# Kernel optimization log

Hardware: AMD Instinct MI355X
Metric: run time of the kernel (lower is better)

Reference implementation:

```python
import jax, jax.numpy as jnp
import numpy as np

B, L, HID = 2, 2048, 2560
H, HKV, DH = 32, 8, 128
G = H // HKV  # GQA groups = 4
EPS = 1e-6
THETA = 1000000.0


def setup_inputs() -> dict:
    key = jax.random.key(0)
    ks = jax.random.split(key, 6)
    x = jax.random.normal(ks[0], (B, L, HID), dtype=jnp.float32)
    Wq = jax.random.normal(ks[1], (HID, H * DH), dtype=jnp.float32) * 0.02
    Wk = jax.random.normal(ks[2], (HID, HKV * DH), dtype=jnp.float32) * 0.02
    Wv = jax.random.normal(ks[3], (HID, HKV * DH), dtype=jnp.float32) * 0.02
    Wo = jax.random.normal(ks[4], (H * DH, HID), dtype=jnp.float32) * 0.02
    q_norm_w = jnp.ones((DH,), dtype=jnp.float32)
    k_norm_w = jnp.ones((DH,), dtype=jnp.float32)
    # RoPE tables, theta=1e6, non-interleaved (half-split) layout
    inv_freq = 1.0 / (THETA ** (jnp.arange(0, DH, 2, dtype=jnp.float32) / DH))
    pos = jnp.arange(L, dtype=jnp.float32)
    freqs = pos[:, None] * inv_freq[None, :]              # [L, DH/2]
    emb = jnp.concatenate([freqs, freqs], axis=-1)        # [L, DH]
    cos = jnp.broadcast_to(jnp.cos(emb)[None], (B, L, DH))
    sin = jnp.broadcast_to(jnp.sin(emb)[None], (B, L, DH))
    return {"x": x, "Wq": Wq, "Wk": Wk, "Wv": Wv, "Wo": Wo,
            "q_norm_w": q_norm_w, "k_norm_w": k_norm_w,
            "cos": cos, "sin": sin}


def _rmsnorm(x, w):
    xf = x.astype(jnp.float32)
    var = jnp.mean(xf * xf, axis=-1, keepdims=True)
    return (xf * jax.lax.rsqrt(var + EPS)).astype(x.dtype) * w


def _rotate_half(x):
    x1, x2 = jnp.split(x, 2, axis=-1)
    return jnp.concatenate([-x2, x1], axis=-1)


def reference(x, Wq, Wk, Wv, Wo, q_norm_w, k_norm_w, cos, sin):
    b, l, _ = x.shape
    q = (x @ Wq).reshape(b, l, H, DH)
    k = (x @ Wk).reshape(b, l, HKV, DH)
    v = (x @ Wv).reshape(b, l, HKV, DH).transpose(0, 2, 1, 3)   # [B,HKV,L,DH]
    q = _rmsnorm(q, q_norm_w).transpose(0, 2, 1, 3)             # [B,H,L,DH]
    k = _rmsnorm(k, k_norm_w).transpose(0, 2, 1, 3)             # [B,HKV,L,DH]
    c = cos[:, None]  # [B,1,L,DH]
    s = sin[:, None]
    q = q * c + _rotate_half(q) * s
    k = k * c + _rotate_half(k) * s
    # GQA SDPA, causal
    qg = q.reshape(b, HKV, G, l, DH)
    scale = 1.0 / np.sqrt(DH)
    scores = jnp.einsum('bkgqd,bkmd->bkgqm', qg, k) * scale     # [B,HKV,G,L,L]
    causal = jnp.tril(jnp.ones((l, l), dtype=bool))
    scores = jnp.where(causal, scores, jnp.finfo(scores.dtype).min)
    attn = jax.nn.softmax(scores, axis=-1)
    out = jnp.einsum('bkgqm,bkmd->bkgqd', attn, v)              # [B,HKV,G,L,DH]
    out = out.reshape(b, H, l, DH).transpose(0, 2, 1, 3).reshape(b, l, H * DH)
    return out @ Wo
```

## Files before the change

kernel.cpp:

```cpp
#include <hip/hip_runtime.h>

typedef unsigned short u16;
typedef unsigned int u32;
using bf16x8 = __attribute__((ext_vector_type(8))) __bf16;
using f32x4  = __attribute__((ext_vector_type(4))) float;

typedef const void __attribute__((address_space(1)))* gas1p;
typedef void __attribute__((address_space(3)))* las3p;

__device__ __forceinline__ void gload16(const void* g, void* l) {
  __builtin_amdgcn_global_load_lds((gas1p)g, (las3p)l, 16, 0, 0);
}

__device__ __forceinline__ u16 f2bf(float f) {
  union { float f; unsigned u; } v; v.f = f;
  unsigned r = v.u + 0x7FFFu + ((v.u >> 16) & 1u);
  return (u16)(r >> 16);
}
__device__ __forceinline__ float bf2f(u16 h) {
  union { unsigned u; float f; } v; v.u = ((unsigned)h) << 16;
  return v.f;
}

__global__ __launch_bounds__(256)
void cvt_f32_bf16(const float4* __restrict__ in, uint2* __restrict__ out, int n4) {
  int i = blockIdx.x * 256 + threadIdx.x;
  if (i >= n4) return;
  float4 v = in[i];
  uint2 o;
  o.x = (unsigned)f2bf(v.x) | ((unsigned)f2bf(v.y) << 16);
  o.y = (unsigned)f2bf(v.z) | ((unsigned)f2bf(v.w) << 16);
  out[i] = o;
}

__global__ __launch_bounds__(256)
void transpose_w(const float* __restrict__ in, u16* __restrict__ out, int R, int C) {
  __shared__ float tile[32][33];
  const int tx = threadIdx.x & 31, ty = threadIdx.x >> 5;
  const int r0 = blockIdx.y * 32, c0 = blockIdx.x * 32;
#pragma unroll
  for (int i = 0; i < 4; i++)
    tile[ty + i * 8][tx] = in[(size_t)(r0 + ty + i * 8) * C + c0 + tx];
  __syncthreads();
#pragma unroll
  for (int i = 0; i < 4; i++)
    out[(size_t)(c0 + ty + i * 8) * R + r0 + tx] = f2bf(tile[tx][ty + i * 8]);
}

__global__ __launch_bounds__(256)
void transpose_v(const u16* __restrict__ QKV, u16* __restrict__ Vt) {
  __shared__ u16 tile[32][34];
  const int tx = threadIdx.x & 31, ty = threadIdx.x >> 5;
  const int l0 = blockIdx.x * 32, d0 = blockIdx.y * 32;
  const int bkv = blockIdx.z;
  const int b = bkv >> 3, kvh = bkv & 7;
#pragma unroll
  for (int i = 0; i < 4; i++)
    tile[ty + i * 8][tx] =
        QKV[(size_t)(b * 2048 + l0 + ty + i * 8) * 6144 + 5120 + kvh * 128 + d0 + tx];
  __syncthreads();
#pragma unroll
  for (int i = 0; i < 4; i++)
    Vt[((size_t)bkv * 128 + d0 + ty + i * 8) * 2048 + l0 + tx] = tile[tx][ty + i * 8];
}

__global__ __launch_bounds__(256)
void norm_rope(const u16* __restrict__ QKV, const float* __restrict__ qw,
               const float* __restrict__ kw, const float* __restrict__ cosp,
               const float* __restrict__ sinp, u16* __restrict__ Qr,
               u16* __restrict__ Kr) {
  const int rid = blockIdx.x * 4 + (threadIdx.x >> 6);
  const int lane = threadIdx.x & 63;
  const int head = rid % 40;
  const int bl = rid / 40;
  const int b = bl >> 11, l = bl & 2047;
  const u16* src; const float* w; u16* dst; float scale;
  if (head < 32) {
    src = QKV + (size_t)bl * 6144 + head * 128;
    w = qw;
    dst = Qr + ((size_t)(b * 32 + head) * 2048 + l) * 128;
    scale = 0.08838834764831845f;
  } else {
    const int kvh = head - 32;
    src = QKV + (size_t)bl * 6144 + 4096 + kvh * 128;
    w = kw;
    dst = Kr + ((size_t)(b * 8 + kvh) * 2048 + l) * 128;
    scale = 1.0f;
  }
  float lo = bf2f(src[lane]);
  float hi = bf2f(src[lane + 64]);
  float ss = lo * lo + hi * hi;
#pragma unroll
  for (int m = 1; m < 64; m <<= 1) ss += __shfl_xor(ss, m, 64);
  const float rstd = rsqrtf(ss * (1.0f / 128.0f) + 1e-6f) * scale;
  const float nlo = lo * rstd * w[lane];
  const float nhi = hi * rstd * w[lane + 64];
  const float* cb = cosp + (size_t)bl * 128;
  const float* sb = sinp + (size_t)bl * 128;
  dst[lane]      = f2bf(nlo * cb[lane]      - nhi * sb[lane]);
  dst[lane + 64] = f2bf(nhi * cb[lane + 64] + nlo * sb[lane + 64]);
}

#define BAR __builtin_amdgcn_s_barrier()
#define WLG { asm volatile("s_waitcnt lgkmcnt(0)" ::: "memory");            \
              __builtin_amdgcn_sched_barrier(0); }
#define WVMn(n) asm volatile("s_waitcnt vmcnt(" #n ")" ::: "memory")
#define SP1 __builtin_amdgcn_s_setprio(1)
#define SP0 __builtin_amdgcn_s_setprio(0)

template <int MI, int NJ, typename CT>
__global__ __launch_bounds__(512, 4)
void gemmK32(const u16* __restrict__ A, const u16* __restrict__ Bt,
             CT* __restrict__ C, int N, int K, int MT) {
  extern __shared__ char smem[];
  constexpr int ASZ = MI * 4096;
  constexpr int BSZ = NJ * 2048;
  constexpr int J1 = (MI == 4) ? 2 : 3;
  const int tid = threadIdx.x, lane = tid & 63, wid = tid >> 6;
  const int wm = wid >> 1, wn = wid & 1;
  const int fr = lane & 15, fq = lane >> 4;
  const int qx = (int)gridDim.x >> 3;
  const int wg = ((int)blockIdx.x & 7) * qx + ((int)blockIdx.x >> 3);
  const int bx = wg / MT, by = wg - bx * MT;
  const int m0 = by * (MI * 64), n0 = bx * (NJ * 32);
  const u16* Ab = A + (size_t)m0 * K;
  const u16* Bb = Bt + (size_t)n0 * K;

  char* const A0 = smem;
  char* const B0 = smem + 2 * ASZ;
#define ABUF(c) (A0 + (c) * ASZ)
#define BBUF(c) (B0 + (c) * BSZ)

  const int sF = (tid >> 2) * K + (tid & 3) * 8;
  const int tq = tid & 255;
  const int sH = (tq >> 2) * K + (tq & 3) * 8;
  const int to = tid & 127;
  const int sO = (to >> 2) * K + (to & 3) * 8;

  const int aRd = (wm * MI * 16 + fr) * 64 + fq * 16;
  const int bRd = (wn * 16 + fr) * 64 + fq * 16;

  f32x4 acc[MI][NJ];
#pragma unroll
  for (int i = 0; i < MI; i++)
#pragma unroll
    for (int j = 0; j < NJ; j++)
#pragma unroll
      for (int r = 0; r < 4; r++) acc[i][j][r] = 0.f;

  bf16x8 af[MI], bfr[3];
  const int NT = K >> 5;

  auto stageP1 = [&](int c2, int kk) {
    if constexpr (MI == 4) {
      gload16(Ab + sF + kk, ABUF(c2) + (tid << 4));
      gload16(Ab + sF + (size_t)128 * K + kk, ABUF(c2) + 8192 + (tid << 4));
    } else {
      gload16(Ab + sF + kk, ABUF(c2) + (tid << 4));
      gload16(Bb + sF + kk, BBUF(c2) + (tid << 4));
    }
  };
  auto stageP2 = [&](int c2, int kk) {
    if constexpr (MI == 4) {
      gload16(Bb + sH + kk, BBUF(c2) + (tq << 4));
      gload16(Bb + sH + (size_t)64 * K + kk, BBUF(c2) + 4096 + (tq << 4));
    } else {
      gload16(Bb + sO + (size_t)128 * K + kk, BBUF(c2) + 8192 + (to << 4));
    }
  };

  stageP1(0, 0);
  stageP2(0, 0);
  WVMn(1);
  BAR;

  for (int t = 0; t < NT; t++) {
    const int c = t & 1, cn = c ^ 1;
    const int kn = ((t + 1 == NT) ? 0 : (t + 1)) << 5;
#pragma unroll
    for (int i = 0; i < MI; i++)
      af[i] = *(const bf16x8*)(ABUF(c) + aRd + i * 1024);
#pragma unroll
    for (int j = 0; j < J1; j++)
      bfr[j] = *(const bf16x8*)(BBUF(c) + bRd + j * 2048);
    stageP1(cn, kn);
    WVMn(2);
    BAR; WLG; SP1;
#pragma unroll
    for (int j = 0; j < J1; j++)
#pragma unroll
      for (int i = 0; i < MI; i++)
        acc[i][j] = __builtin_amdgcn_mfma_f32_16x16x32_bf16(af[i], bfr[j], acc[i][j], 0, 0, 0);
    SP0; BAR;
#pragma unroll
    for (int j = J1; j < NJ; j++)
      bfr[j - J1] = *(const bf16x8*)(BBUF(c) + bRd + j * 2048);
    stageP2(cn, kn);
    WVMn(1);
    BAR; WLG; SP1;
#pragma unroll
    for (int j = J1; j < NJ; j++)
#pragma unroll
      for (int i = 0; i < MI; i++)
        acc[i][j] = __builtin_amdgcn_mfma_f32_16x16x32_bf16(af[i], bfr[j - J1], acc[i][j], 0, 0, 0);
    SP0; BAR;
  }
  WVMn(0);

#pragma unroll
  for (int i = 0; i < MI; i++) {
    const int row0 = m0 + (wm * MI + i) * 16 + fq * 4;
#pragma unroll
    for (int j = 0; j < NJ; j++) {
      const int col = n0 + (j * 2 + wn) * 16 + fr;
#pragma unroll
      for (int r = 0; r < 4; r++) {
        const size_t idx = (size_t)(row0 + r) * N + col;
        if constexpr (sizeof(CT) == 2) C[idx] = f2bf(acc[i][j][r]);
        else C[idx] = acc[i][j][r];
      }
    }
  }
#undef ABUF
#undef BBUF
}

__global__ __launch_bounds__(256, 2)
void attn_fwd(const u16* __restrict__ Qr, const u16* __restrict__ Kr,
              const u16* __restrict__ Vt, u16* __restrict__ AO) {
  const int L = 2048, DH = 128;
  __shared__ u16 Ks[2][64 * 128];
  __shared__ u16 Vs[2][128 * 64];
  const int tid = threadIdx.x, lane = tid & 63, wid = tid >> 6;
  const int fr = lane & 15, fq = lane >> 4;
  const int j = blockIdx.x >> 4;
  const int grp = blockIdx.x & 15;
  const int kvh = grp >> 1, b = grp & 1;
  const int h = kvh * 4 + wid;

  const u16* Kbase = Kr + (size_t)(b * 8 + kvh) * L * DH;
  const u16* Vbase = Vt + (size_t)(b * 8 + kvh) * DH * L;

  int Dly[4], kOff[4], vOff[4];
#pragma unroll
  for (int p = 0; p < 4; p++) {
    const int D = (tid + p * 256) * 16;
    Dly[p] = D;
    const int kr = D >> 8, kc = ((D >> 4) & 15) ^ (kr & 7);
    kOff[p] = kr * 128 + kc * 8;
    const int vr = D >> 7, vc = ((D >> 4) & 7) ^ (vr & 7);
    vOff[p] = vr * 2048 + vc * 8;
  }

  const bool B5 = (lane & 32) != 0;
  const bool A4 = (lane & 16) != 0;

  auto stage = [&](int kt, int bufi) {
    const int k0 = kt * 64;
#pragma unroll
    for (int p = 0; p < 4; p++) {
      gload16(Kbase + (size_t)k0 * 128 + kOff[p], (char*)&Ks[bufi][0] + Dly[p]);
      gload16(Vbase + k0 + vOff[p], (char*)&Vs[bufi][0] + Dly[p]);
    }
  };

  for (int half = 0; half < 2; half++) {
    const int t = half ? 63 - j : j;
    const int nk = (t >> 1) + 1;

    bf16x8 qf[2][4];
#pragma unroll
    for (int g = 0; g < 2; g++) {
      const int qq = t * 32 + g * 16 + fr;
      const u16* qbase = Qr + ((size_t)(b * 32 + h) * L + qq) * DH + fq * 8;
#pragma unroll
      for (int dt = 0; dt < 4; dt++) qf[g][dt] = *(const bf16x8*)(qbase + dt * 32);
    }
    asm volatile("s_waitcnt vmcnt(0)" ::: "memory");

    f32x4 o[2][8];
#pragma unroll
    for (int g = 0; g < 2; g++)
#pragma unroll
      for (int d = 0; d < 8; d++)
#pragma unroll
        for (int r = 0; r < 4; r++) o[g][d][r] = 0.f;
    float mrow[2] = {-__builtin_huge_valf(), -__builtin_huge_valf()};
    float lrow[2] = {0.f, 0.f};

    __builtin_amdgcn_s_barrier();
    stage(0, 0);
    int cur = 0;

    for (int kt = 0; kt < nk; kt++) {
      if (kt + 1 < nk) {
        stage(kt + 1, cur ^ 1);
        asm volatile("s_waitcnt vmcnt(8)" ::: "memory");
      } else {
        asm volatile("s_waitcnt vmcnt(0)" ::: "memory");
      }
      __builtin_amdgcn_s_barrier();

      const u16* KsB = &Ks[cur][0];
      const u16* VsB = &Vs[cur][0];
      const int k0 = kt * 64;

      f32x4 s4[2][4];
#pragma unroll
      for (int g = 0; g < 2; g++)
#pragma unroll
        for (int ni = 0; ni < 4; ni++)
#pragma unroll
          for (int r = 0; r < 4; r++) s4[g][ni][r] = 0.f;
#pragma unroll
      for (int ni = 0; ni < 4; ni++) {
        const int krow = ni * 16 + fr;
        const int sw = (krow & 7) << 4;
#pragma unroll
        for (int dt = 0; dt < 4; dt++) {
          const int off = (krow * 256 + dt * 64 + fq * 16) ^ sw;
          bf16x8 kf = *(const bf16x8*)((const char*)KsB + off);
          s4[0][ni] = __builtin_amdgcn_mfma_f32_16x16x32_bf16(kf, qf[0][dt], s4[0][ni], 0, 0, 0);
          s4[1][ni] = __builtin_amdgcn_mfma_f32_16x16x32_bf16(kf, qf[1][dt], s4[1][ni], 0, 0, 0);
        }
      }

      if (kt == nk - 1) {
#pragma unroll
        for (int g = 0; g < 2; g++) {
          const int qq = t * 32 + g * 16 + fr;
#pragma unroll
          for (int ni = 0; ni < 4; ni++)
#pragma unroll
            for (int r = 0; r < 4; r++)
              if (k0 + ni * 16 + fq * 4 + r > qq) s4[g][ni][r] = -1e30f;
        }
      }

      bf16x8 pb[2][2];
#pragma unroll
      for (int g = 0; g < 2; g++) {
        float mt = s4[g][0][0];
#pragma unroll
        for (int ni = 0; ni < 4; ni++)
#pragma unroll
          for (int r = 0; r < 4; r++) mt = fmaxf(mt, s4[g][ni][r]);
        mt = fmaxf(mt, __shfl_xor(mt, 16, 64));
        mt = fmaxf(mt, __shfl_xor(mt, 32, 64));

        if (!__all(mt <= mrow[g] + 8.f)) {
          const float mn = fmaxf(mrow[g], mt);
          const float corr = exp2f((mrow[g] - mn) * 1.44269504f);
          mrow[g] = mn;
          lrow[g] *= corr;
#pragma unroll
          for (int d = 0; d < 8; d++)
#pragma unroll
            for (int r = 0; r < 4; r++) o[g][d][r] *= corr;
        }

        const float ml = mrow[g] * 1.44269504f;
        float rs = 0.f;
#pragma unroll
        for (int ni = 0; ni < 4; ni++)
#pragma unroll
          for (int r = 0; r < 4; r++) {
            const float pv = exp2f(fmaf(s4[g][ni][r], 1.44269504f, -ml));
            s4[g][ni][r] = pv;
            rs += pv;
          }
        rs += __shfl_xor(rs, 16, 64);
        rs += __shfl_xor(rs, 32, 64);
        lrow[g] += rs;

        u32 pk[4][2];
#pragma unroll
        for (int ni = 0; ni < 4; ni++) {
          pk[ni][0] = __builtin_amdgcn_perm(__float_as_uint(s4[g][ni][1]),
                                            __float_as_uint(s4[g][ni][0]), 0x07060302u);
          pk[ni][1] = __builtin_amdgcn_perm(__float_as_uint(s4[g][ni][3]),
                                            __float_as_uint(s4[g][ni][2]), 0x07060302u);
        }
#pragma unroll
        for (int ks = 0; ks < 2; ks++) {
          u32 r00 = pk[2 * ks + 0][0], r01 = pk[2 * ks + 0][1];
          u32 r10 = pk[2 * ks + 1][0], r11 = pk[2 * ks + 1][1];
          u32 e0 = __shfl_xor(B5 ? r00 : r10, 32, 64);
          u32 t00 = B5 ? e0 : r00, t10 = B5 ? r10 : e0;
          u32 e1 = __shfl_xor(B5 ? r01 : r11, 32, 64);
          u32 t01 = B5 ? e1 : r01, t11 = B5 ? r11 : e1;
          u32 e2 = __shfl_xor(A4 ? t00 : t10, 16, 64);
          u32 u00 = A4 ? e2 : t00, u10 = A4 ? t10 : e2;
          u32 e3 = __shfl_xor(A4 ? t01 : t11, 16, 64);
          u32 u01 = A4 ? e3 : t01, u11 = A4 ? t11 : e3;
          union { u32 u[4]; bf16x8 v; } pbv;
          pbv.u[0] = u00; pbv.u[1] = u01; pbv.u[2] = u10; pbv.u[3] = u11;
          pb[g][ks] = pbv.v;
        }
      }

#pragma unroll
      for (int d = 0; d < 8; d++) {
        const int vrow = d * 16 + fr;
        const int sw = (vrow & 7) << 4;
#pragma unroll
        for (int ks = 0; ks < 2; ks++) {
          const int off = (vrow * 128 + ks * 64 + fq * 16) ^ sw;
          bf16x8 vf = *(const bf16x8*)((const char*)VsB + off);
          o[0][d] = __builtin_amdgcn_mfma_f32_16x16x32_bf16(vf, pb[0][ks], o[0][d], 0, 0, 0);
          o[1][d] = __builtin_amdgcn_mfma_f32_16x16x32_bf16(vf, pb[1][ks], o[1][d], 0, 0, 0);
        }
      }
      __builtin_amdgcn_s_barrier();
      cur ^= 1;
    }

#pragma unroll
    for (int g = 0; g < 2; g++) {
      const float inv = 1.f / lrow[g];
      const int qq = t * 32 + g * 16 + fr;
      u16* obase = AO + ((size_t)b * L + qq) * 4096 + h * 128 + fq * 4;
#pragma unroll
      for (int d = 0; d < 8; d++) {
        uint2 w;
        w.x = (u32)f2bf(o[g][d][0] * inv) | ((u32)f2bf(o[g][d][1] * inv) << 16);
        w.y = (u32)f2bf(o[g][d][2] * inv) | ((u32)f2bf(o[g][d][3] * inv) << 16);
        *(uint2*)(obase + d * 16) = w;
      }
    }
  }
}

extern "C" void kernel_launch(void* const* d_in, const int* in_sizes, int n_in,
                              void* d_out, int out_size, void* d_ws, size_t ws_size,
                              hipStream_t stream) {
  const float* x    = (const float*)d_in[0];
  const float* Wq   = (const float*)d_in[1];
  const float* Wk   = (const float*)d_in[2];
  const float* Wv   = (const float*)d_in[3];
  const float* Wo   = (const float*)d_in[4];
  const float* qw   = (const float*)d_in[5];
  const float* kw   = (const float*)d_in[6];
  const float* cosp = (const float*)d_in[7];
  const float* sinp = (const float*)d_in[8];
  float* out = (float*)d_out;
  char* ws = (char*)d_ws;

  u16* xb    = (u16*)(ws);
  u16* WqkvT = (u16*)(ws + 20971520);
  u16* WoT   = (u16*)(ws + 52428800);
  u16* QKV   = (u16*)(ws + 73400320);
  u16* AO    = QKV;
  u16* Qrr   = (u16*)(ws + 123731968);
  u16* Krr   = (u16*)(ws + 157286400);
  u16* Vtt   = (u16*)(ws + 165675008);

  hipFuncSetAttribute(reinterpret_cast<const void*>(&gemmK32<4, 4, u16>),
                      hipFuncAttributeMaxDynamicSharedMemorySize, 49152);
  hipFuncSetAttribute(reinterpret_cast<const void*>(&gemmK32<2, 5, float>),
                      hipFuncAttributeMaxDynamicSharedMemorySize, 36864);

  cvt_f32_bf16<<<10240, 256, 0, stream>>>((const float4*)x, (uint2*)xb, 2621440);
  transpose_w<<<dim3(128, 80), 256, 0, stream>>>(Wq, WqkvT, 2560, 4096);
  transpose_w<<<dim3(32, 80), 256, 0, stream>>>(Wk, WqkvT + (size_t)4096 * 2560, 2560, 1024);
  transpose_w<<<dim3(32, 80), 256, 0, stream>>>(Wv, WqkvT + (size_t)5120 * 2560, 2560, 1024);
  transpose_w<<<dim3(80, 128), 256, 0, stream>>>(Wo, WoT, 4096, 2560);

  gemmK32<4, 4, u16><<<768, 512, 49152, stream>>>(xb, WqkvT, QKV, 6144, 2560, 16);

  norm_rope<<<40960, 256, 0, stream>>>(QKV, qw, kw, cosp, sinp, Qrr, Krr);
  transpose_v<<<dim3(64, 4, 16), 256, 0, stream>>>(QKV, Vtt);

  attn_fwd<<<dim3(512), 256, 0, stream>>>(Qrr, Krr, Vtt, AO);

  gemmK32<2, 5, float><<<512, 512, 36864, stream>>>(AO, WoT, out, 2560, 4096, 32);
}
```

Baseline: 470.1 us.

## Rewrite GEMM with K=64 tiles, XOR-swizzled LDS, and two-ahead prefetch

Replaces the K=32 split-phase GEMM with a templated kernel that stages K=64 slices into XOR-swizzled shared memory, which is meant to avoid LDS bank conflicts. It prefetches two tiles ahead into a double buffer and runs both k-substeps per barrier pair. Tile shapes change for both projections: QKV now uses 128x192 tiles with a 2x4 warp grid, and the output GEMM uses 128x160 tiles. The aim is fewer barriers per unit of work and better LDS read efficiency. In exchange it needs more shared memory per block, which may lower occupancy.

```diff
diff --git a/kernel.cpp b/kernel.cpp
--- a/kernel.cpp
+++ b/kernel.cpp
@@ -108,102 +108,98 @@
 #define SP1 __builtin_amdgcn_s_setprio(1)
 #define SP0 __builtin_amdgcn_s_setprio(0)
 
-template <int MI, int NJ, typename CT>
+template <int BM, int BN, int WM, int WN, typename CT>
 __global__ __launch_bounds__(512, 4)
-void gemmK32(const u16* __restrict__ A, const u16* __restrict__ Bt,
-             CT* __restrict__ C, int N, int K, int MT) {
+void gemmT(const u16* __restrict__ A, const u16* __restrict__ Bt,
+           CT* __restrict__ C, int N, int K, int MT) {
   extern __shared__ char smem[];
-  constexpr int ASZ = MI * 4096;
-  constexpr int BSZ = NJ * 2048;
-  constexpr int J1 = (MI == 4) ? 2 : 3;
+  constexpr int ASZ = BM * 128;
+  constexpr int BSZ = BN * 128;
+  constexpr int MI = BM / WM / 16;
+  constexpr int NJF = BN / WN / 16;
   const int tid = threadIdx.x, lane = tid & 63, wid = tid >> 6;
-  const int wm = wid >> 1, wn = wid & 1;
+  const int wm = wid / WN, wn = wid % WN;
   const int fr = lane & 15, fq = lane >> 4;
   const int qx = (int)gridDim.x >> 3;
   const int wg = ((int)blockIdx.x & 7) * qx + ((int)blockIdx.x >> 3);
   const int bx = wg / MT, by = wg - bx * MT;
-  const int m0 = by * (MI * 64), n0 = bx * (NJ * 32);
+  const int m0 = by * BM, n0 = bx * BN;
   const u16* Ab = A + (size_t)m0 * K;
   const u16* Bb = Bt + (size_t)n0 * K;
 
-  char* const A0 = smem;
-  char* const B0 = smem + 2 * ASZ;
-#define ABUF(c) (A0 + (c) * ASZ)
-#define BBUF(c) (B0 + (c) * BSZ)
-
-  const int sF = (tid >> 2) * K + (tid & 3) * 8;
-  const int tq = tid & 255;
-  const int sH = (tq >> 2) * K + (tq & 3) * 8;
-  const int to = tid & 127;
-  const int sO = (to >> 2) * K + (to & 3) * 8;
-
-  const int aRd = (wm * MI * 16 + fr) * 64 + fq * 16;
-  const int bRd = (wn * 16 + fr) * 64 + fq * 16;
-
-  f32x4 acc[MI][NJ];
+#define ABUF(c) (smem + (c) * ASZ)
+#define BBUF(c) (smem + 2 * ASZ + (c) * BSZ)
+
+  f32x4 acc[MI][NJF];
 #pragma unroll
   for (int i = 0; i < MI; i++)
 #pragma unroll
-    for (int j = 0; j < NJ; j++)
+    for (int j = 0; j < NJF; j++)
 #pragma unroll
       for (int r = 0; r < 4; r++) acc[i][j][r] = 0.f;
 
-  bf16x8 af[MI], bfr[3];
-  const int NT = K >> 5;
-
-  auto stageP1 = [&](int c2, int kk) {
-    if constexpr (MI == 4) {
-      gload16(Ab + sF + kk, ABUF(c2) + (tid << 4));
-      gload16(Ab + sF + (size_t)128 * K + kk, ABUF(c2) + 8192 + (tid << 4));
-    } else {
-      gload16(Ab + sF + kk, ABUF(c2) + (tid << 4));
-      gload16(Bb + sF + kk, BBUF(c2) + (tid << 4));
+  auto stage = [&](int c, int kk) {
+#pragma unroll
+    for (int l = 0; l < BM / 64; l++) {
+      const int u = tid + 512 * l, row = u >> 3, ch = u & 7;
+      gload16(Ab + (size_t)row * K + ((ch ^ (row & 7)) << 3) + kk,
+              ABUF(c) + (u << 4));
+    }
+#pragma unroll
+    for (int l = 0; l < BN / 64; l++) {
+      const int u = tid + 512 * l, row = u >> 3, ch = u & 7;
+      gload16(Bb + (size_t)row * K + ((ch ^ (row & 7)) << 3) + kk,
+              BBUF(c) + (u << 4));
+    }
+    if constexpr ((BN % 64) != 0) {
+      const int u = (BN / 64) * 512 + (tid & 255), row = u >> 3, ch = u & 7;
+      gload16(Bb + (size_t)row * K + ((ch ^ (row & 7)) << 3) + kk,
+              BBUF(c) + (u << 4));
     }
   };
-  auto stageP2 = [&](int c2, int kk) {
-    if constexpr (MI == 4) {
-      gload16(Bb + sH + kk, BBUF(c2) + (tq << 4));
-      gload16(Bb + sH + (size_t)64 * K + kk, BBUF(c2) + 4096 + (tq << 4));
-    } else {
-      gload16(Bb + sO + (size_t)128 * K + kk, BBUF(c2) + 8192 + (to << 4));
-    }
-  };
-
-  stageP1(0, 0);
-  stageP2(0, 0);
-  WVMn(1);
+
+  const int NT = K >> 6;
+  stage(0, 0);
+  stage(1, 64);
+  WVMn(5);
   BAR;
 
+  bf16x8 af[MI][2], bf[NJF][2];
   for (int t = 0; t < NT; t++) {
-    const int c = t & 1, cn = c ^ 1;
-    const int kn = ((t + 1 == NT) ? 0 : (t + 1)) << 5;
-#pragma unroll
-    for (int i = 0; i < MI; i++)
-      af[i] = *(const bf16x8*)(ABUF(c) + aRd + i * 1024);
-#pragma unroll
-    for (int j = 0; j < J1; j++)
-      bfr[j] = *(const bf16x8*)(BBUF(c) + bRd + j * 2048);
-    stageP1(cn, kn);
-    WVMn(2);
-    BAR; WLG; SP1;
-#pragma unroll
-    for (int j = 0; j < J1; j++)
-#pragma unroll
-      for (int i = 0; i < MI; i++)
-        acc[i][j] = __builtin_amdgcn_mfma_f32_16x16x32_bf16(af[i], bfr[j], acc[i][j], 0, 0, 0);
-    SP0; BAR;
-#pragma unroll
-    for (int j = J1; j < NJ; j++)
-      bfr[j - J1] = *(const bf16x8*)(BBUF(c) + bRd + j * 2048);
-    stageP2(cn, kn);
-    WVMn(1);
-    BAR; WLG; SP1;
-#pragma unroll
-    for (int j = J1; j < NJ; j++)
-#pragma unroll
-      for (int i = 0; i < MI; i++)
-        acc[i][j] = __builtin_amdgcn_mfma_f32_16x16x32_bf16(af[i], bfr[j - J1], acc[i][j], 0, 0, 0);
-    SP0; BAR;
+    const int c = t & 1;
+#pragma unroll
+    for (int i = 0; i < MI; i++) {
+      const int row = (wm * MI + i) * 16 + fr;
+#pragma unroll
+      for (int ks = 0; ks < 2; ks++)
+        af[i][ks] = *(const bf16x8*)(ABUF(c) + row * 128 +
+                                     ((((ks << 2) + fq) ^ (row & 7)) << 4));
+    }
+#pragma unroll
+    for (int j = 0; j < NJF; j++) {
+      const int row = (j * WN + wn) * 16 + fr;
+#pragma unroll
+      for (int ks = 0; ks < 2; ks++)
+        bf[j][ks] = *(const bf16x8*)(BBUF(c) + row * 128 +
+                                     ((((ks << 2) + fq) ^ (row & 7)) << 4));
+    }
+    WLG;
+    BAR;
+    int t2 = t + 2; if (t2 >= NT) t2 -= NT;
+    stage(c, t2 << 6);
+    WVMn(5);
+    SP1;
+#pragma unroll
+    for (int j = 0; j < NJF; j++)
+#pragma unroll
+      for (int i = 0; i < MI; i++) {
+        acc[i][j] = __builtin_amdgcn_mfma_f32_16x16x32_bf16(af[i][0], bf[j][0],
+                                                            acc[i][j], 0, 0, 0);
+        acc[i][j] = __builtin_amdgcn_mfma_f32_16x16x32_bf16(af[i][1], bf[j][1],
+                                                            acc[i][j], 0, 0, 0);
+      }
+    SP0;
+    BAR;
   }
   WVMn(0);
 
@@ -211,8 +207,8 @@
   for (int i = 0; i < MI; i++) {
     const int row0 = m0 + (wm * MI + i) * 16 + fq * 4;
 #pragma unroll
-    for (int j = 0; j < NJ; j++) {
-      const int col = n0 + (j * 2 + wn) * 16 + fr;
+    for (int j = 0; j < NJF; j++) {
+      const int col = n0 + (j * WN + wn) * 16 + fr;
 #pragma unroll
       for (int r = 0; r < 4; r++) {
         const size_t idx = (size_t)(row0 + r) * N + col;
@@ -455,10 +451,10 @@
   u16* Krr   = (u16*)(ws + 157286400);
   u16* Vtt   = (u16*)(ws + 165675008);
 
-  hipFuncSetAttribute(reinterpret_cast<const void*>(&gemmK32<4, 4, u16>),
-                      hipFuncAttributeMaxDynamicSharedMemorySize, 49152);
-  hipFuncSetAttribute(reinterpret_cast<const void*>(&gemmK32<2, 5, float>),
-                      hipFuncAttributeMaxDynamicSharedMemorySize, 36864);
+  hipFuncSetAttribute(reinterpret_cast<const void*>(&gemmT<128, 192, 2, 4, u16>),
+                      hipFuncAttributeMaxDynamicSharedMemorySize, 81920);
+  hipFuncSetAttribute(reinterpret_cast<const void*>(&gemmT<128, 160, 4, 2, float>),
+                      hipFuncAttributeMaxDynamicSharedMemorySize, 73728);
 
   cvt_f32_bf16<<<10240, 256, 0, stream>>>((const float4*)x, (uint2*)xb, 2621440);
   transpose_w<<<dim3(128, 80), 256, 0, stream>>>(Wq, WqkvT, 2560, 4096);
@@ -466,12 +462,12 @@
   transpose_w<<<dim3(32, 80), 256, 0, stream>>>(Wv, WqkvT + (size_t)5120 * 2560, 2560, 1024);
   transpose_w<<<dim3(80, 128), 256, 0, stream>>>(Wo, WoT, 4096, 2560);
 
-  gemmK32<4, 4, u16><<<768, 512, 49152, stream>>>(xb, WqkvT, QKV, 6144, 2560, 16);
+  gemmT<128, 192, 2, 4, u16><<<1024, 512, 81920, stream>>>(xb, WqkvT, QKV, 6144, 2560, 32);
 
   norm_rope<<<40960, 256, 0, stream>>>(QKV, qw, kw, cosp, sinp, Qrr, Krr);
   transpose_v<<<dim3(64, 4, 16), 256, 0, stream>>>(QKV, Vtt);
 
   attn_fwd<<<dim3(512), 256, 0, stream>>>(Qrr, Krr, Vtt, AO);
 
-  gemmK32<2, 5, float><<<512, 512, 36864, stream>>>(AO, WoT, out, 2560, 4096, 32);
-}
+  gemmT<128, 160, 4, 2, float><<<512, 512, 73728, stream>>>(AO, WoT, out, 2560, 4096, 32);
+}
```

Result: faster. 424.5 us (-9.7%).
